# Optimization experiments

Hardware: AMD Instinct MI355X
Metric: run time of the kernel (lower is better)

Reference implementation:

```python
import jax, jax.numpy as jnp
import numpy as np

N_NODES = 100000


def gcn_conv(x, W, b, src, dst, n_nodes):
    # PyG GCNConv: h = x @ W; add self-loops; norm = d^-1/2[src] * d^-1/2[dst];
    # aggregate sum of norm * h[src] at dst; then + bias.
    h = x @ W  # [N, F_out]
    loops = jnp.arange(n_nodes, dtype=src.dtype)
    s = jnp.concatenate([src, loops])  # [E+N]
    d = jnp.concatenate([dst, loops])
    deg = jax.ops.segment_sum(jnp.ones_like(d, dtype=h.dtype), d, num_segments=n_nodes)
    dinv = jax.lax.rsqrt(deg)  # deg >= 1 thanks to self-loops
    norm = dinv[s] * dinv[d]  # [E+N]
    msg = h[s] * norm[:, None]  # [E+N, F_out] -- large gather
    out = jax.ops.segment_sum(msg, d, num_segments=n_nodes)  # scatter-add
    return out + b


def setup_inputs() -> dict:
    key = jax.random.key(0)
    k = jax.random.split(key, 8)
    x = jax.random.normal(k[0], (N_NODES, 8), dtype=jnp.float32)
    edge_index = jax.random.randint(k[1], (2, 1600000), 0, N_NODES, dtype=jnp.int32)
    W1 = jax.random.normal(k[2], (8, 64), dtype=jnp.float32) * 0.3
    b1 = jnp.zeros((64,), dtype=jnp.float32)
    W2 = jax.random.normal(k[3], (64, 128), dtype=jnp.float32) * 0.1
    b2 = jnp.zeros((128,), dtype=jnp.float32)
    Wfc = jax.random.normal(k[4], (128, 1), dtype=jnp.float32) * 0.08
    bfc = jnp.zeros((1,), dtype=jnp.float32)
    return {"x": x, "edge_index": edge_index, "W1": W1, "b1": b1,
            "W2": W2, "b2": b2, "Wfc": Wfc, "bfc": bfc}


def reference(x, edge_index, W1, b1, W2, b2, Wfc, bfc):
    src, dst = edge_index[0], edge_index[1]
    n = x.shape[0]
    h = jax.nn.relu(gcn_conv(x, W1, b1, src, dst, n))   # dropout: eval mode (identity)
    h = jax.nn.relu(gcn_conv(h, W2, b2, src, dst, n))
    g = jnp.mean(h, axis=0)  # [128] graph readout
    return g @ Wfc + bfc     # [1]
```

## Files before the change

kernel.cpp:

```cpp
#include <hip/hip_runtime.h>


#define CHUNK 4096
#define NB_SHIFT 8
#define BCAP 5120
#define G2_GRID 1042

typedef float v2f __attribute__((ext_vector_type(2)));
typedef __bf16 bf16x8 __attribute__((ext_vector_type(8)));
typedef float f32x16 __attribute__((ext_vector_type(16)));

__device__ __forceinline__ unsigned short f2bf(float f) {
    unsigned u = __float_as_uint(f);
    return (unsigned short)((u + 0x7fffu + ((u >> 16) & 1u)) >> 16);
}
__device__ __forceinline__ unsigned pkbf(float a, float b) {
    return ((unsigned)f2bf(b) << 16) | f2bf(a);
}
__device__ __forceinline__ float bflo(unsigned u) { return __uint_as_float(u << 16); }
__device__ __forceinline__ float bfhi(unsigned u) { return __uint_as_float(u & 0xffff0000u); }
__device__ __forceinline__ bf16x8 asbf8(uint4 v) { return __builtin_bit_cast(bf16x8, v); }

__global__ void scatterA(const int* __restrict__ ei, int E, int* __restrict__ cursor,
                         unsigned int* __restrict__ bucketed) {
    __shared__ unsigned int pk[CHUNK];
    __shared__ unsigned short bk[CHUNK];
    __shared__ unsigned int spk[CHUNK];
    __shared__ unsigned short sbk[CHUNK];
    __shared__ int h[512], hsc[512], lcur[512], rbase[512];
    int tid = threadIdx.x;
    h[tid] = 0;
    h[tid + 256] = 0;
    lcur[tid] = 0;
    lcur[tid + 256] = 0;
    __syncthreads();
    int cbase = blockIdx.x * CHUNK;
    int cN = min(CHUNK, E - cbase);
    const int* src = ei;
    const int* dst = ei + E;
    for (int i = tid; i < cN; i += 256) {
        int s = src[cbase + i], d = dst[cbase + i];
        int b = d >> NB_SHIFT;
        pk[i] = (unsigned)s | ((unsigned)(d & 255) << 17);
        bk[i] = (unsigned short)b;
        atomicAdd(&h[b], 1);
    }
    __syncthreads();
    hsc[tid] = h[tid];
    hsc[tid + 256] = h[tid + 256];
    __syncthreads();
    for (int off = 1; off < 512; off <<= 1) {
        int v0 = (tid >= off) ? hsc[tid - off] : 0;
        int v1 = (tid + 256 >= off) ? hsc[tid + 256 - off] : 0;
        __syncthreads();
        hsc[tid] += v0;
        hsc[tid + 256] += v1;
        __syncthreads();
    }
    hsc[tid] -= h[tid];
    hsc[tid + 256] -= h[tid + 256];
#pragma unroll
    for (int k = 0; k < 2; k++) {
        int i = tid + k * 256;
        if (h[i]) rbase[i] = i * BCAP + atomicAdd(&cursor[i], h[i]);
    }
    __syncthreads();
    for (int i = tid; i < cN; i += 256) {
        int b = bk[i];
        int pos = hsc[b] + atomicAdd(&lcur[b], 1);
        spk[pos] = pk[i];
        sbk[pos] = (unsigned short)b;
    }
    __syncthreads();
    for (int p = tid; p < cN; p += 256) {
        int b = sbk[p];
        bucketed[rbase[b] + (p - hsc[b])] = spk[p];
    }
}

__global__ void buildB(const unsigned int* __restrict__ bucketed,
                       const int* __restrict__ cursor, int* __restrict__ row_start,
                       int* __restrict__ cntg, float* __restrict__ dinv,
                       int* __restrict__ csr_src, const float* __restrict__ x,
                       unsigned int* __restrict__ xsb, int n) {
    __shared__ unsigned int spk[BCAP];
    __shared__ int scsr[BCAP];
    __shared__ int cnt[256], sc[256], cur[256];
    __shared__ float sdinv[256];
    int tid = threadIdx.x;
    int b = blockIdx.x;
    int s0 = b * BCAP;
    int m = cursor[b];
    cnt[tid] = 0;
    __syncthreads();
    for (int e = tid; e < m; e += 256) {
        unsigned v = bucketed[s0 + e];
        spk[e] = v;
        atomicAdd(&cnt[v >> 17], 1);
    }
    __syncthreads();
    sc[tid] = cnt[tid];
    __syncthreads();
    for (int off = 1; off < 256; off <<= 1) {
        int v0 = (tid >= off) ? sc[tid - off] : 0;
        __syncthreads();
        sc[tid] += v0;
        __syncthreads();
    }
    int nb0 = b << NB_SHIFT;
    int node = nb0 + tid;
    int ex = sc[tid] - cnt[tid];
    cur[tid] = ex;
    float dv = rsqrtf((float)cnt[tid] + 1.0f);
    sdinv[tid] = dv;
    if (node < n) {
        row_start[node] = s0 + ex;
        cntg[node] = cnt[tid];
        dinv[node] = dv;
    }
    __syncthreads();
    for (int e = tid; e < m; e += 256) {
        unsigned v = spk[e];
        int r = atomicAdd(&cur[v >> 17], 1);
        scsr[r] = (int)(v & 0x1FFFFu);
    }
    __syncthreads();
    for (int e = tid; e < m; e += 256) csr_src[s0 + e] = scsr[e];
    int lim = min(n - nb0, 256) * 4;
    for (int i = tid; i < lim; i += 256) {
        float2 v = ((const float2*)x)[nb0 * 4 + i];
        float dvv = sdinv[i >> 2];
        xsb[nb0 * 4 + i] = pkbf(v.x * dvv, v.y * dvv);
    }
}

__global__ __launch_bounds__(256) void aggX_gemm1(
    const unsigned int* __restrict__ xsb, const float* __restrict__ dinv,
    const int* __restrict__ row_start, const int* __restrict__ cnt,
    const int* __restrict__ csr_src, const float* __restrict__ W1,
    const float* __restrict__ b1, unsigned int* __restrict__ h1q, int n) {
    __shared__ float w[512 + 64];
    __shared__ float axl[64 * 8];
    __shared__ float sdi[64];
    int tid = threadIdx.x;
    for (int i = tid; i < 512; i += 256) w[i] = W1[i];
    if (tid < 64) w[512 + tid] = b1[tid];
    int g = tid >> 2, l = tid & 3;
    int node = blockIdx.x * 64 + g;
    float a[8] = {};
    float di = 0.f;
    if (node < n) {
        di = dinv[node];
        const uint4* xs4 = (const uint4*)xsb;
        int e0 = row_start[node], e1 = e0 + cnt[node];
        int e = e0 + l;
        for (; e + 4 < e1; e += 8) {
            int sA = csr_src[e], sB = csr_src[e + 4];
            uint4 uA = xs4[sA], uB = xs4[sB];
            a[0] += bflo(uA.x) + bflo(uB.x);
            a[1] += bfhi(uA.x) + bfhi(uB.x);
            a[2] += bflo(uA.y) + bflo(uB.y);
            a[3] += bfhi(uA.y) + bfhi(uB.y);
            a[4] += bflo(uA.z) + bflo(uB.z);
            a[5] += bfhi(uA.z) + bfhi(uB.z);
            a[6] += bflo(uA.w) + bflo(uB.w);
            a[7] += bfhi(uA.w) + bfhi(uB.w);
        }
        for (; e < e1; e += 4) {
            uint4 u = xs4[csr_src[e]];
            a[0] += bflo(u.x); a[1] += bfhi(u.x);
            a[2] += bflo(u.y); a[3] += bfhi(u.y);
            a[4] += bflo(u.z); a[5] += bfhi(u.z);
            a[6] += bflo(u.w); a[7] += bfhi(u.w);
        }
        if (l == 0) {
            uint4 u = xs4[node];
            a[0] += bflo(u.x); a[1] += bfhi(u.x);
            a[2] += bflo(u.y); a[3] += bfhi(u.y);
            a[4] += bflo(u.z); a[5] += bfhi(u.z);
            a[6] += bflo(u.w); a[7] += bfhi(u.w);
        }
    }
#pragma unroll
    for (int k = 0; k < 8; k++) {
        a[k] += __shfl_xor(a[k], 1);
        a[k] += __shfl_xor(a[k], 2);
    }
    axl[g * 8 + 2 * l] = di * a[2 * l];
    axl[g * 8 + 2 * l + 1] = di * a[2 * l + 1];
    if (l == 0) sdi[g] = di;
    __syncthreads();
    int wv = tid >> 6, lane = tid & 63;
    int nb = blockIdx.x * 64;
    for (int it = 0; it < 16; it++) {
        int nl = wv * 16 + it;
        int nd = nb + nl;
        if (nd >= n) break;
        float h = w[512 + lane];
#pragma unroll
        for (int k = 0; k < 8; k++) h = fmaf(axl[nl * 8 + k], w[k * 64 + lane], h);
        float h1s = fmaxf(h, 0.f) * sdi[nl];
        unsigned word = ((unsigned)__builtin_amdgcn_cvt_pk_fp8_f32(h1s, h1s, 0, false)
                         & 0xFFu) << ((lane & 3) * 8);
        word |= __shfl_xor((int)word, 1);
        word |= __shfl_xor((int)word, 2);
        if ((lane & 3) == 0) h1q[nd * 16 + (lane >> 2)] = word;
    }
}

__global__ void agg64(const unsigned int* __restrict__ h1q, const float* __restrict__ dinv,
                      const int* __restrict__ row_start, const int* __restrict__ cnt,
                      const int* __restrict__ csr_src, uint2* __restrict__ ahb, int n) {
    int gid = blockIdx.x * blockDim.x + threadIdx.x;
    int node = gid >> 4;
    if (node >= n) return;
    int cq = threadIdx.x & 15;
    int es = cq >> 2, qp = cq & 3;
    const uint4* h4 = (const uint4*)h1q;
    float a[16] = {};
    int e0 = row_start[node], e1 = e0 + cnt[node];
    int e = e0 + es;
    for (; e + 4 < e1; e += 8) {
        int sA = csr_src[e], sB = csr_src[e + 4];
        uint4 uA = h4[sA * 4 + qp], uB = h4[sB * 4 + qp];
#pragma unroll
        for (int wdx = 0; wdx < 4; wdx++) {
            unsigned wa = (&uA.x)[wdx], wb = (&uB.x)[wdx];
            v2f la = __builtin_amdgcn_cvt_pk_f32_fp8((int)wa, false);
            v2f ha = __builtin_amdgcn_cvt_pk_f32_fp8((int)wa, true);
            v2f lb = __builtin_amdgcn_cvt_pk_f32_fp8((int)wb, false);
            v2f hb = __builtin_amdgcn_cvt_pk_f32_fp8((int)wb, true);
            a[wdx * 4 + 0] += la[0] + lb[0];
            a[wdx * 4 + 1] += la[1] + lb[1];
            a[wdx * 4 + 2] += ha[0] + hb[0];
            a[wdx * 4 + 3] += ha[1] + hb[1];
        }
    }
    for (; e < e1; e += 4) {
        uint4 u = h4[csr_src[e] * 4 + qp];
#pragma unroll
        for (int wdx = 0; wdx < 4; wdx++) {
            unsigned wu = (&u.x)[wdx];
            v2f lo = __builtin_amdgcn_cvt_pk_f32_fp8((int)wu, false);
            v2f hi = __builtin_amdgcn_cvt_pk_f32_fp8((int)wu, true);
            a[wdx * 4 + 0] += lo[0];
            a[wdx * 4 + 1] += lo[1];
            a[wdx * 4 + 2] += hi[0];
            a[wdx * 4 + 3] += hi[1];
        }
    }
    if (es == 0) {
        uint4 u = h4[node * 4 + qp];
#pragma unroll
        for (int wdx = 0; wdx < 4; wdx++) {
            unsigned wu = (&u.x)[wdx];
            v2f lo = __builtin_amdgcn_cvt_pk_f32_fp8((int)wu, false);
            v2f hi = __builtin_amdgcn_cvt_pk_f32_fp8((int)wu, true);
            a[wdx * 4 + 0] += lo[0];
            a[wdx * 4 + 1] += lo[1];
            a[wdx * 4 + 2] += hi[0];
            a[wdx * 4 + 3] += hi[1];
        }
    }
#pragma unroll
    for (int k = 0; k < 16; k++) {
        a[k] += __shfl_xor(a[k], 4);
        a[k] += __shfl_xor(a[k], 8);
    }
    if (es == 0) {
        float di = dinv[node];
        uint4 r0, r1;
        r0.x = pkbf(di * a[0], di * a[1]);
        r0.y = pkbf(di * a[2], di * a[3]);
        r0.z = pkbf(di * a[4], di * a[5]);
        r0.w = pkbf(di * a[6], di * a[7]);
        r1.x = pkbf(di * a[8], di * a[9]);
        r1.y = pkbf(di * a[10], di * a[11]);
        r1.z = pkbf(di * a[12], di * a[13]);
        r1.w = pkbf(di * a[14], di * a[15]);
        uint4* out4 = (uint4*)ahb;
        out4[node * 8 + qp * 2] = r0;
        out4[node * 8 + qp * 2 + 1] = r1;
    }
}

__global__ __launch_bounds__(256) void gemm2_fused(
    const uint2* __restrict__ ahb, const float* __restrict__ W2,
    const float* __restrict__ b2, float* __restrict__ partial, int n) {
    __shared__ __align__(16) uint4 wb4[4 * 4 * 64];
    __shared__ __align__(16) uint4 atp4[32 * 8];
    int tid = threadIdx.x;
    unsigned* wbd = (unsigned*)wb4;
    for (int i = tid; i < 4096; i += 256) {
        int j = i & 127;
        int r = i >> 7;
        int t = r >> 3, l5s = (r >> 2) & 1, d = r & 3;
        int k0 = 16 * t + 8 * l5s + 2 * d;
        unsigned val = pkbf(W2[k0 * 128 + j], W2[(k0 + 1) * 128 + j]);
        int w = j >> 5, lan = l5s * 32 + (j & 31);
        wbd[(((w * 4 + t) * 64) + lan) * 4 + d] = val;
    }
    int lane = tid & 63;
    int w = tid >> 6;
    int col = lane & 31;
    int l5 = lane >> 5;
    float bj = b2[w * 32 + col];
    const uint4* ahb4 = (const uint4*)ahb;
    float colsum = 0.f;
    int ntiles = (n + 31) >> 5;
    for (int tt = blockIdx.x; tt < ntiles; tt += gridDim.x) {
        int base = tt * 32;
        __syncthreads();
        {
            int nl = tid >> 3, s = tid & 7;
            uint4 v = make_uint4(0u, 0u, 0u, 0u);
            if (base + nl < n) v = ahb4[(base + nl) * 8 + s];
            atp4[nl * 8 + (s ^ (nl & 7))] = v;
        }
        __syncthreads();
        f32x16 acc = {};
#pragma unroll
        for (int t = 0; t < 4; t++) {
            int s = 2 * t + l5;
            uint4 av = atp4[col * 8 + (s ^ (col & 7))];
            uint4 bv = wb4[(w * 4 + t) * 64 + lane];
            acc = __builtin_amdgcn_mfma_f32_32x32x16_bf16(asbf8(av), asbf8(bv), acc,
                                                          0, 0, 0);
        }
        int nvalid = n - base;
#pragma unroll
        for (int reg = 0; reg < 16; reg++) {
            int row = (reg & 3) + 8 * (reg >> 2) + 4 * l5;
            if (row < nvalid) colsum += fmaxf(acc[reg] + bj, 0.f);
        }
    }
    colsum += __shfl_xor(colsum, 32);
    if (l5 == 0) partial[blockIdx.x * 128 + w * 32 + col] = colsum;
}

__global__ __launch_bounds__(1024) void finish_kernel(
    const float* __restrict__ partial, const float* __restrict__ Wfc,
    const float* __restrict__ bfc, float* __restrict__ out, float invN) {
    __shared__ float sh[1024 + 2];
    int tid = threadIdx.x;
    int c = tid & 127, g = tid >> 7;
    float s = 0.f;
#pragma unroll 8
    for (int b = g; b < G2_GRID; b += 8) s += partial[b * 128 + c];
    sh[tid] = s;
    __syncthreads();
    if (tid < 512) sh[tid] += sh[tid + 512];
    __syncthreads();
    if (tid < 256) sh[tid] += sh[tid + 256];
    __syncthreads();
    if (tid < 128) {
        float v = (sh[tid] + sh[tid + 128]) * Wfc[tid];
#pragma unroll
        for (int off = 32; off > 0; off >>= 1) v += __shfl_down(v, off);
        if ((tid & 63) == 0) sh[1024 + (tid >> 6)] = v;
    }
    __syncthreads();
    if (tid == 0) out[0] = (sh[1024] + sh[1025]) * invN + bfc[0];
}

extern "C" void kernel_launch(void* const* d_in, const int* in_sizes, int n_in,
                              void* d_out, int out_size, void* d_ws, size_t ws_size,
                              hipStream_t stream) {
    const float* x   = (const float*)d_in[0];
    const int* ei    = (const int*)d_in[1];
    const float* W1  = (const float*)d_in[2];
    const float* b1  = (const float*)d_in[3];
    const float* W2  = (const float*)d_in[4];
    const float* b2  = (const float*)d_in[5];
    const float* Wfc = (const float*)d_in[6];
    const float* bfc = (const float*)d_in[7];
    float* out = (float*)d_out;

    const int n = in_sizes[0] / 8;
    const int E = in_sizes[1] / 2;

    const int nA = (E + CHUNK - 1) / CHUNK;
    const int B = (n + 255) >> NB_SHIFT;

    char* ws = (char*)d_ws;
    size_t off = 0;
    auto alloc = [&](size_t bytes) -> char* {
        char* p = ws + off;
        off = (off + bytes + 255) & ~(size_t)255;
        return p;
    };
    int*            cursor    = (int*)alloc(512 * 4);
    unsigned int*   bucketed  = (unsigned int*)alloc((size_t)B * BCAP * 4);
    int*            row_start = (int*)alloc((size_t)n * 4);
    int*            cnt       = (int*)alloc((size_t)n * 4);
    float*          dinv      = (float*)alloc((size_t)n * 4);
    int*            csr_src   = (int*)alloc((size_t)B * BCAP * 4);
    unsigned int*   xsb       = (unsigned int*)alloc((size_t)n * 16);
    unsigned int*   h1q       = (unsigned int*)alloc((size_t)n * 64);
    uint2*          ahb       = (uint2*)alloc((size_t)n * 128);
    float*          partial   = (float*)alloc((size_t)G2_GRID * 128 * 4);
    (void)ws_size;

    hipMemsetAsync(cursor, 0, 512 * 4, stream);
    scatterA<<<nA, 256, 0, stream>>>(ei, E, cursor, bucketed);
    buildB<<<B, 256, 0, stream>>>(bucketed, cursor, row_start, cnt, dinv, csr_src,
                                  x, xsb, n);
    aggX_gemm1<<<(n + 63) / 64, 256, 0, stream>>>(xsb, dinv, row_start, cnt, csr_src,
                                                  W1, b1, h1q, n);
    agg64<<<(n * 16 + 255) / 256, 256, 0, stream>>>(h1q, dinv, row_start, cnt, csr_src,
                                                    ahb, n);
    gemm2_fused<<<G2_GRID, 256, 0, stream>>>(ahb, W2, b2, partial, n);
    finish_kernel<<<1, 1024, 0, stream>>>(partial, Wfc, bfc, out, 1.0f / (float)n);
}
```

Before: 168.1 us.

## Use 512-thread blocks for bucketing kernels and hoist W2 fragments into registers

scatterA and buildB now launch with 512 threads per block, so each thread handles half as many edges in the histogram, scatter and CSR build loops. In buildB the extra threads sit idle during the 256-entry prefix scan. gemm2_fused adds a barrier after staging W2, then loads its four B-operand fragments into registers once instead of reading shared memory every tile. Its row-validity check is skipped for full 32-row tiles. The larger blocks may lower occupancy because of the heavy shared-memory use per block.

```diff
diff --git a/kernel.cpp b/kernel.cpp
--- a/kernel.cpp
+++ b/kernel.cpp
@@ -21,8 +21,9 @@
 __device__ __forceinline__ float bfhi(unsigned u) { return __uint_as_float(u & 0xffff0000u); }
 __device__ __forceinline__ bf16x8 asbf8(uint4 v) { return __builtin_bit_cast(bf16x8, v); }
 
-__global__ void scatterA(const int* __restrict__ ei, int E, int* __restrict__ cursor,
-                         unsigned int* __restrict__ bucketed) {
+__global__ __launch_bounds__(512) void scatterA(const int* __restrict__ ei, int E,
+                                                int* __restrict__ cursor,
+                                                unsigned int* __restrict__ bucketed) {
     __shared__ unsigned int pk[CHUNK];
     __shared__ unsigned short bk[CHUNK];
     __shared__ unsigned int spk[CHUNK];
@@ -30,15 +31,13 @@
     __shared__ int h[512], hsc[512], lcur[512], rbase[512];
     int tid = threadIdx.x;
     h[tid] = 0;
-    h[tid + 256] = 0;
     lcur[tid] = 0;
-    lcur[tid + 256] = 0;
     __syncthreads();
     int cbase = blockIdx.x * CHUNK;
     int cN = min(CHUNK, E - cbase);
     const int* src = ei;
     const int* dst = ei + E;
-    for (int i = tid; i < cN; i += 256) {
+    for (int i = tid; i < cN; i += 512) {
         int s = src[cbase + i], d = dst[cbase + i];
         int b = d >> NB_SHIFT;
         pk[i] = (unsigned)s | ((unsigned)(d & 255) << 17);
@@ -47,42 +46,34 @@
     }
     __syncthreads();
     hsc[tid] = h[tid];
-    hsc[tid + 256] = h[tid + 256];
     __syncthreads();
     for (int off = 1; off < 512; off <<= 1) {
         int v0 = (tid >= off) ? hsc[tid - off] : 0;
-        int v1 = (tid + 256 >= off) ? hsc[tid + 256 - off] : 0;
         __syncthreads();
         hsc[tid] += v0;
-        hsc[tid + 256] += v1;
         __syncthreads();
     }
     hsc[tid] -= h[tid];
-    hsc[tid + 256] -= h[tid + 256];
-#pragma unroll
-    for (int k = 0; k < 2; k++) {
-        int i = tid + k * 256;
-        if (h[i]) rbase[i] = i * BCAP + atomicAdd(&cursor[i], h[i]);
-    }
-    __syncthreads();
-    for (int i = tid; i < cN; i += 256) {
+    if (h[tid]) rbase[tid] = tid * BCAP + atomicAdd(&cursor[tid], h[tid]);
+    __syncthreads();
+    for (int i = tid; i < cN; i += 512) {
         int b = bk[i];
         int pos = hsc[b] + atomicAdd(&lcur[b], 1);
         spk[pos] = pk[i];
         sbk[pos] = (unsigned short)b;
     }
     __syncthreads();
-    for (int p = tid; p < cN; p += 256) {
+    for (int p = tid; p < cN; p += 512) {
         int b = sbk[p];
         bucketed[rbase[b] + (p - hsc[b])] = spk[p];
     }
 }
 
-__global__ void buildB(const unsigned int* __restrict__ bucketed,
-                       const int* __restrict__ cursor, int* __restrict__ row_start,
-                       int* __restrict__ cntg, float* __restrict__ dinv,
-                       int* __restrict__ csr_src, const float* __restrict__ x,
-                       unsigned int* __restrict__ xsb, int n) {
+__global__ __launch_bounds__(512) void buildB(
+    const unsigned int* __restrict__ bucketed, const int* __restrict__ cursor,
+    int* __restrict__ row_start, int* __restrict__ cntg, float* __restrict__ dinv,
+    int* __restrict__ csr_src, const float* __restrict__ x,
+    unsigned int* __restrict__ xsb, int n) {
     __shared__ unsigned int spk[BCAP];
     __shared__ int scsr[BCAP];
     __shared__ int cnt[256], sc[256], cur[256];
@@ -91,43 +82,45 @@
     int b = blockIdx.x;
     int s0 = b * BCAP;
     int m = cursor[b];
-    cnt[tid] = 0;
-    __syncthreads();
-    for (int e = tid; e < m; e += 256) {
+    if (tid < 256) cnt[tid] = 0;
+    __syncthreads();
+    for (int e = tid; e < m; e += 512) {
         unsigned v = bucketed[s0 + e];
         spk[e] = v;
         atomicAdd(&cnt[v >> 17], 1);
     }
     __syncthreads();
-    sc[tid] = cnt[tid];
+    if (tid < 256) sc[tid] = cnt[tid];
     __syncthreads();
     for (int off = 1; off < 256; off <<= 1) {
-        int v0 = (tid >= off) ? sc[tid - off] : 0;
-        __syncthreads();
-        sc[tid] += v0;
+        int v0 = (tid < 256 && tid >= off) ? sc[tid - off] : 0;
+        __syncthreads();
+        if (tid < 256) sc[tid] += v0;
         __syncthreads();
     }
     int nb0 = b << NB_SHIFT;
-    int node = nb0 + tid;
-    int ex = sc[tid] - cnt[tid];
-    cur[tid] = ex;
-    float dv = rsqrtf((float)cnt[tid] + 1.0f);
-    sdinv[tid] = dv;
-    if (node < n) {
-        row_start[node] = s0 + ex;
-        cntg[node] = cnt[tid];
-        dinv[node] = dv;
-    }
-    __syncthreads();
-    for (int e = tid; e < m; e += 256) {
+    if (tid < 256) {
+        int node = nb0 + tid;
+        int ex = sc[tid] - cnt[tid];
+        cur[tid] = ex;
+        float dv = rsqrtf((float)cnt[tid] + 1.0f);
+        sdinv[tid] = dv;
+        if (node < n) {
+            row_start[node] = s0 + ex;
+            cntg[node] = cnt[tid];
+            dinv[node] = dv;
+        }
+    }
+    __syncthreads();
+    for (int e = tid; e < m; e += 512) {
         unsigned v = spk[e];
         int r = atomicAdd(&cur[v >> 17], 1);
         scsr[r] = (int)(v & 0x1FFFFu);
     }
     __syncthreads();
-    for (int e = tid; e < m; e += 256) csr_src[s0 + e] = scsr[e];
+    for (int e = tid; e < m; e += 512) csr_src[s0 + e] = scsr[e];
     int lim = min(n - nb0, 256) * 4;
-    for (int i = tid; i < lim; i += 256) {
+    for (int i = tid; i < lim; i += 512) {
         float2 v = ((const float2*)x)[nb0 * 4 + i];
         float dvv = sdinv[i >> 2];
         xsb[nb0 * 4 + i] = pkbf(v.x * dvv, v.y * dvv);
@@ -300,10 +293,15 @@
         int w = j >> 5, lan = l5s * 32 + (j & 31);
         wbd[(((w * 4 + t) * 64) + lan) * 4 + d] = val;
     }
+    __syncthreads();
     int lane = tid & 63;
     int w = tid >> 6;
     int col = lane & 31;
     int l5 = lane >> 5;
+    uint4 bf0 = wb4[(w * 4 + 0) * 64 + lane];
+    uint4 bf1 = wb4[(w * 4 + 1) * 64 + lane];
+    uint4 bf2 = wb4[(w * 4 + 2) * 64 + lane];
+    uint4 bf3 = wb4[(w * 4 + 3) * 64 + lane];
     float bj = b2[w * 32 + col];
     const uint4* ahb4 = (const uint4*)ahb;
     float colsum = 0.f;
@@ -319,19 +317,26 @@
         }
         __syncthreads();
         f32x16 acc = {};
-#pragma unroll
-        for (int t = 0; t < 4; t++) {
-            int s = 2 * t + l5;
-            uint4 av = atp4[col * 8 + (s ^ (col & 7))];
-            uint4 bv = wb4[(w * 4 + t) * 64 + lane];
-            acc = __builtin_amdgcn_mfma_f32_32x32x16_bf16(asbf8(av), asbf8(bv), acc,
-                                                          0, 0, 0);
+        {
+            uint4 a0 = atp4[col * 8 + ((2 * 0 + l5) ^ (col & 7))];
+            acc = __builtin_amdgcn_mfma_f32_32x32x16_bf16(asbf8(a0), asbf8(bf0), acc, 0, 0, 0);
+            uint4 a1 = atp4[col * 8 + ((2 * 1 + l5) ^ (col & 7))];
+            acc = __builtin_amdgcn_mfma_f32_32x32x16_bf16(asbf8(a1), asbf8(bf1), acc, 0, 0, 0);
+            uint4 a2 = atp4[col * 8 + ((2 * 2 + l5) ^ (col & 7))];
+            acc = __builtin_amdgcn_mfma_f32_32x32x16_bf16(asbf8(a2), asbf8(bf2), acc, 0, 0, 0);
+            uint4 a3 = atp4[col * 8 + ((2 * 3 + l5) ^ (col & 7))];
+            acc = __builtin_amdgcn_mfma_f32_32x32x16_bf16(asbf8(a3), asbf8(bf3), acc, 0, 0, 0);
         }
         int nvalid = n - base;
-#pragma unroll
-        for (int reg = 0; reg < 16; reg++) {
-            int row = (reg & 3) + 8 * (reg >> 2) + 4 * l5;
-            if (row < nvalid) colsum += fmaxf(acc[reg] + bj, 0.f);
+        if (nvalid >= 32) {
+#pragma unroll
+            for (int reg = 0; reg < 16; reg++) colsum += fmaxf(acc[reg] + bj, 0.f);
+        } else {
+#pragma unroll
+            for (int reg = 0; reg < 16; reg++) {
+                int rrow = (reg & 3) + 8 * (reg >> 2) + 4 * l5;
+                if (rrow < nvalid) colsum += fmaxf(acc[reg] + bj, 0.f);
+            }
         }
     }
     colsum += __shfl_xor(colsum, 32);
@@ -402,8 +407,8 @@
     (void)ws_size;
 
     hipMemsetAsync(cursor, 0, 512 * 4, stream);
-    scatterA<<<nA, 256, 0, stream>>>(ei, E, cursor, bucketed);
-    buildB<<<B, 256, 0, stream>>>(bucketed, cursor, row_start, cnt, dinv, csr_src,
+    scatterA<<<nA, 512, 0, stream>>>(ei, E, cursor, bucketed);
+    buildB<<<B, 512, 0, stream>>>(bucketed, cursor, row_start, cnt, dinv, csr_src,
                                   x, xsb, n);
     aggX_gemm1<<<(n + 63) / 64, 256, 0, stream>>>(xsb, dinv, row_start, cnt, csr_src,
                                                   W1, b1, h1q, n);
```

After: 162.7 us. 3.2% less time.
